# Performance work log

Hardware: AMD Instinct MI355X
Metric: run time of the kernel (lower is better)

The kernel has to match this reference:

```python
import jax, jax.numpy as jnp
import numpy as np

CONF_THR = 0.2      # confidence_threshold default
NMS_THR = 0.45      # nms_threshold default
TARGET_ID = 0       # NAME2ID['person'] in COCO ordering
CLASS_OFFSET = 1e4  # per-class box offset so cross-class IoU == 0 (per-class NMS)
B, N, C = 4, 8192, 80


def setup_inputs() -> dict:
    key = jax.random.key(0)
    kxy, kwh, kobj, kcls = jax.random.split(key, 4)
    xy = jax.random.uniform(kxy, (B, N, 2)) * 600.0          # x1, y1
    wh = jax.random.uniform(kwh, (B, N, 2)) * 100.0 + 1.0    # box w, h
    boxes = jnp.concatenate([xy, xy + wh], axis=-1)           # x1 y1 x2 y2
    obj = jax.random.uniform(kobj, (B, N, 1))                 # objectness score
    clsp = jax.random.uniform(kcls, (B, N, C))                # class probs
    detection = jnp.concatenate([boxes, obj, clsp], axis=-1)  # [B, N, 5+C]
    return {"detection": detection}


def _pairwise_iou(b):
    # b: [N, 4] in x1y1x2y2
    area = (b[:, 2] - b[:, 0]) * (b[:, 3] - b[:, 1])
    lt = jnp.maximum(b[:, None, :2], b[None, :, :2])
    rb = jnp.minimum(b[:, None, 2:], b[None, :, 2:])
    wh = jnp.clip(rb - lt, 0.0)
    inter = wh[..., 0] * wh[..., 1]
    return inter / (area[:, None] + area[None, :] - inter + 1e-9)


def _nms_image(boxes, scores, classprobs, labels):
    # Fixed-shape, masked equivalent of the torch per-image filter+per-class NMS.
    valid = (scores > CONF_THR) & (labels == TARGET_ID)
    s = jnp.where(valid, scores, -1.0)
    order = jnp.argsort(-s)  # descending score (NMS visiting order)
    b = boxes[order]
    s = s[order]
    cp = classprobs[order]
    lb = labels[order]
    v = valid[order]
    # Offset boxes per class label -> IoU between different classes is 0,
    # which exactly reproduces the per-class NMS loop.
    ob = b + lb.astype(b.dtype)[:, None] * CLASS_OFFSET
    iou = _pairwise_iou(ob)  # [N, N]

    def step(keep, xs):
        row, i, vi = xs
        suppressed = jnp.any(keep & (row > NMS_THR))
        k = vi & jnp.logical_not(suppressed)
        return keep.at[i].set(k), k

    _, keep = jax.lax.scan(
        step, jnp.zeros(s.shape[0], dtype=bool), (iou, jnp.arange(s.shape[0]), v)
    )
    # Compact kept detections to the front (stable sort preserves descending score
    # order among kept boxes, matching the final argsort in torch).
    s_rank = jnp.where(keep, s, -1.0)
    final = jnp.argsort(-s_rank)
    kf = keep[final]
    m = kf.astype(b.dtype)
    out_boxes = b[final] * m[:, None]
    out_scores = jnp.where(kf, s[final], 0.0)
    out_classprobs = cp[final] * m
    out_labels = jnp.where(kf, lb[final], -1)
    return out_boxes, out_scores, out_classprobs, out_labels


def reference(detection):
    # split_detections
    boxes = detection[..., :4]           # [B, N, 4]
    scores = detection[..., 4]           # [B, N]
    cls = detection[..., 5:]             # [B, N, C]
    classprobs = jnp.max(cls, axis=-1)
    labels = jnp.argmax(cls, axis=-1)
    # filter_detections, batched over images
    return jax.vmap(_nms_image)(boxes, scores, classprobs, labels)
```

## Files before the change

### kernel.cpp

```cpp
#include <hip/hip_runtime.h>
#include <cstdint>
#include <cstddef>

typedef unsigned long long u64;

#define BB 4
#define NN 8192
#define DSTRIDE 85
#define RPB 64
#define BPI 128
#define NBLK (BB * BPI)
#define RCAP 64
#define SCAP 192
#define CONF_THRF 0.2f
#define NMS_THRF 0.45f
#define PLANE (BB * NN)

__device__ __forceinline__ void wave_fence() {
  __asm__ volatile("s_waitcnt lgkmcnt(0)" ::: "memory");
  __builtin_amdgcn_wave_barrier();
}

__global__ __launch_bounds__(256) void scan_kernel(
    const float* __restrict__ det, float* __restrict__ out,
    int* __restrict__ counts, float* __restrict__ cand) {
  __shared__ int wcnt[4];
  const int tid = threadIdx.x;
  const int blk = blockIdx.x;
  const int r = tid >> 2, q = tid & 3;
  const int row = blk * RPB + r;
  const float* d = det + (size_t)row * DSTRIDE;

  float best = -1.0f; int barg = 0;
  const float* cb = d + 5 + 20 * q;
#pragma unroll
  for (int k = 0; k < 5; ++k) {
    float4 v = *reinterpret_cast<const float4*>(cb + 4 * k);
    int c0 = 20 * q + 4 * k;
    if (v.x > best) { best = v.x; barg = c0; }
    if (v.y > best) { best = v.y; barg = c0 + 1; }
    if (v.z > best) { best = v.z; barg = c0 + 2; }
    if (v.w > best) { best = v.w; barg = c0 + 3; }
  }
#pragma unroll
  for (int off = 1; off <= 2; off <<= 1) {
    float ov = __shfl_xor(best, off);
    int   oa = __shfl_xor(barg, off);
    if (ov > best || (ov == best && oa < barg)) { best = ov; barg = oa; }
  }

  float4 box = make_float4(0.f, 0.f, 0.f, 0.f);
  float score = 0.f;
  bool valid = false;
  if (q == 0) {
    box = *reinterpret_cast<const float4*>(d);
    score = d[4];
    valid = (score > CONF_THRF) && (barg == 0);
  }

  const int base = blk * RPB;
  if (tid < 64) {
    reinterpret_cast<float4*>(out)[base + tid] = make_float4(0.f, 0.f, 0.f, 0.f);
  } else if (tid < 128) {
    out[(size_t)PLANE * 4 + base + (tid - 64)] = 0.f;
  } else if (tid < 192) {
    out[(size_t)PLANE * 5 + base + (tid - 128)] = 0.f;
  } else {
    out[(size_t)PLANE * 6 + base + (tid - 192)] = -1.0f;
  }

  u64 mask = __ballot(valid);
  const int wave = tid >> 6, lane = tid & 63;
  if (lane == 0) wcnt[wave] = __popcll(mask);
  __syncthreads();
  if (valid) {
    int offw = (wave > 0 ? wcnt[0] : 0) + (wave > 1 ? wcnt[1] : 0) +
               (wave > 2 ? wcnt[2] : 0);
    int pos = __popcll(mask & ((1ull << lane) - 1ull));
    float* p = cand + ((size_t)blk * RCAP + (offw + pos)) * 8;
    reinterpret_cast<float4*>(p)[0] = box;
    reinterpret_cast<float4*>(p)[1] =
        make_float4(score, best, __int_as_float(row & (NN - 1)), 0.f);
  }
  if (tid == 0) counts[blk] = wcnt[0] + wcnt[1] + wcnt[2] + wcnt[3];
}

__global__ __launch_bounds__(64) void nms_kernel(
    float* __restrict__ out, const int* __restrict__ counts,
    const float* __restrict__ cand) {
  __shared__ u64 keys[SCAP];
  __shared__ u64 mat[SCAP * 3];
  __shared__ float ux1[SCAP], uy1[SCAP], ux2[SCAP], uy2[SCAP];
  __shared__ float usc[SCAP], ucp[SCAP];
  __shared__ float sx1[SCAP], sy1[SCAP], sx2[SCAP], sy2[SCAP];
  __shared__ float sar[SCAP], ssc[SCAP], scp[SCAP];

  const int img = blockIdx.x;
  const int lane = threadIdx.x;

  const int m0 = img * BPI + lane, m1 = m0 + 64;
  int c0 = counts[m0];
  int c1 = counts[m1];

  int s0 = c0;
#pragma unroll
  for (int d = 1; d < 64; d <<= 1) {
    int t = __shfl_up(s0, d);
    if (lane >= d) s0 += t;
  }
  int tot0 = __shfl(s0, 63);
  int s1 = c1;
#pragma unroll
  for (int d = 1; d < 64; d <<= 1) {
    int t = __shfl_up(s1, d);
    if (lane >= d) s1 += t;
  }
  s1 += tot0;
  int K = __shfl(s1, 63);
  if (K > SCAP) K = SCAP;
  int e0 = s0 - c0, e1 = s1 - c1;

#pragma unroll
  for (int pass = 0; pass < 2; ++pass) {
    int m = pass ? m1 : m0;
    int c = pass ? c1 : c0;
    int e = pass ? e1 : e0;
    const float4* p =
        reinterpret_cast<const float4*>(cand + (size_t)m * RCAP * 8);
    for (int k = 0; k < c; ++k) {
      int o = e + k;
      if (o < SCAP) {
        float4 a = p[2 * k], bq = p[2 * k + 1];
        ux1[o] = a.x; uy1[o] = a.y; ux2[o] = a.z; uy2[o] = a.w;
        usc[o] = bq.x; ucp[o] = bq.y;
        int idx = __float_as_int(bq.z);
        keys[o] = ((u64)__float_as_uint(bq.x) << 32) |
                  ((u64)(unsigned)(0xFFFF - idx) << 16) | (unsigned)o;
      }
    }
  }
  wave_fence();

  for (int o = lane; o < K; o += 64) {
    u64 my = keys[o];
    int rr = 0;
    for (int s = 0; s < K; ++s) rr += (keys[s] > my) ? 1 : 0;
    float x1 = ux1[o], y1 = uy1[o], x2 = ux2[o], y2 = uy2[o];
    sx1[rr] = x1; sy1[rr] = y1; sx2[rr] = x2; sy2[rr] = y2;
    sar[rr] = (x2 - x1) * (y2 - y1);
    ssc[rr] = usc[o]; scp[rr] = ucp[o];
  }
  wave_fence();

  for (int i = lane; i < K; i += 64) {
    float ax1 = sx1[i], ay1 = sy1[i], ax2 = sx2[i], ay2 = sy2[i], aa = sar[i];
    u64 w0 = 0, w1 = 0, w2 = 0;
    for (int j = i + 1; j < K; ++j) {
      float xx1 = fmaxf(ax1, sx1[j]);
      float yy1 = fmaxf(ay1, sy1[j]);
      float xx2 = fminf(ax2, sx2[j]);
      float yy2 = fminf(ay2, sy2[j]);
      float w = fmaxf(xx2 - xx1, 0.f);
      float h = fmaxf(yy2 - yy1, 0.f);
      float inter = w * h;
      float iou = inter / (aa + sar[j] - inter + 1e-9f);
      if (iou > NMS_THRF) {
        u64 bit = 1ull << (j & 63);
        int wj = j >> 6;
        w0 |= (wj == 0) ? bit : 0;
        w1 |= (wj == 1) ? bit : 0;
        w2 |= (wj == 2) ? bit : 0;
      }
    }
    mat[i * 3] = w0; mat[i * 3 + 1] = w1; mat[i * 3 + 2] = w2;
  }
  wave_fence();

  u64 rem0 = 0, rem1 = 0, rem2 = 0, kp0 = 0, kp1 = 0, kp2 = 0;
#define GREEDY_CHUNK(WW, REMW, KPW)                                      \
  for (int ii = 0; ii < 64; ++ii) {                                      \
    int i = (WW) * 64 + ii;                                              \
    if (i >= K) break;                                                   \
    u64 g0 = mat[i * 3], g1 = mat[i * 3 + 1], g2 = mat[i * 3 + 2];       \
    if (!((REMW >> ii) & 1ull)) {                                        \
      KPW |= 1ull << ii;                                                 \
      rem0 |= g0; rem1 |= g1; rem2 |= g2;                                \
    }                                                                    \
  }
  GREEDY_CHUNK(0, rem0, kp0)
  GREEDY_CHUNK(1, rem1, kp1)
  GREEDY_CHUNK(2, rem2, kp2)
#undef GREEDY_CHUNK

  for (int i = lane; i < K; i += 64) {
    int wi = i >> 6, bi = i & 63;
    u64 kw = (wi == 0) ? kp0 : (wi == 1) ? kp1 : kp2;
    if ((kw >> bi) & 1ull) {
      int rr = (wi > 0 ? __popcll(kp0) : 0) + (wi > 1 ? __popcll(kp1) : 0) +
               __popcll(kw & ((1ull << bi) - 1ull));
      size_t o = (size_t)img * NN + rr;
      reinterpret_cast<float4*>(out)[o] =
          make_float4(sx1[i], sy1[i], sx2[i], sy2[i]);
      out[(size_t)PLANE * 4 + o] = ssc[i];
      out[(size_t)PLANE * 5 + o] = scp[i];
      out[(size_t)PLANE * 6 + o] = 0.0f;
    }
  }
}

extern "C" void kernel_launch(void* const* d_in, const int* in_sizes, int n_in,
                              void* d_out, int out_size, void* d_ws, size_t ws_size,
                              hipStream_t stream) {
  const float* det = (const float*)d_in[0];
  float* out = (float*)d_out;
  int* counts = (int*)d_ws;
  float* cand = (float*)((char*)d_ws + 2048);

  scan_kernel<<<NBLK, 256, 0, stream>>>(det, out, counts, cand);
  nms_kernel<<<BB, 64, 0, stream>>>(out, counts, cand);
}
```

Baseline: 87.12 us.

## Stage detection rows in LDS with coalesced float4 loads, halve rows per block

The scan kernel now copies each block's contiguous slab of 32 detection rows into shared memory with fully coalesced float4 loads, then runs the per-row class argmax from LDS using 8 threads per row. Before, each thread read unaligned float4s directly from the 85-float-stride rows. Rows per block drop from 64 to 32, so the block count doubles to 1024, and the NMS kernel scans and gathers four count segments instead of two. This trades an extra LDS round trip and a barrier for better global-load coalescing and more parallelism. It also adds more candidate segments for the single-wave NMS gather to walk.

Result: slower. 89.57 us (+2.8%).

```diff
diff --git a/kernel.cpp b/kernel.cpp
--- a/kernel.cpp
+++ b/kernel.cpp
@@ -7,10 +7,10 @@
 #define BB 4
 #define NN 8192
 #define DSTRIDE 85
-#define RPB 64
-#define BPI 128
+#define RPB 32
+#define BPI 256
 #define NBLK (BB * BPI)
-#define RCAP 64
+#define RCAP 32
 #define SCAP 192
 #define CONF_THRF 0.2f
 #define NMS_THRF 0.45f
@@ -24,26 +24,33 @@
 __global__ __launch_bounds__(256) void scan_kernel(
     const float* __restrict__ det, float* __restrict__ out,
     int* __restrict__ counts, float* __restrict__ cand) {
+  __shared__ __align__(16) float st[RPB * DSTRIDE];
   __shared__ int wcnt[4];
   const int tid = threadIdx.x;
   const int blk = blockIdx.x;
-  const int r = tid >> 2, q = tid & 3;
-  const int row = blk * RPB + r;
-  const float* d = det + (size_t)row * DSTRIDE;
-
+
+  {
+    const float4* src =
+        reinterpret_cast<const float4*>(det + (size_t)blk * (RPB * DSTRIDE));
+    float4* dst = reinterpret_cast<float4*>(st);
+#pragma unroll
+    for (int i = 0; i < 3; ++i) {
+      int idx = tid + 256 * i;
+      if (idx < (RPB * DSTRIDE) / 4) dst[idx] = src[idx];
+    }
+  }
+  __syncthreads();
+
+  const int r = tid >> 3, o = tid & 7;
+  const float* rowp = st + r * DSTRIDE;
   float best = -1.0f; int barg = 0;
-  const float* cb = d + 5 + 20 * q;
 #pragma unroll
-  for (int k = 0; k < 5; ++k) {
-    float4 v = *reinterpret_cast<const float4*>(cb + 4 * k);
-    int c0 = 20 * q + 4 * k;
-    if (v.x > best) { best = v.x; barg = c0; }
-    if (v.y > best) { best = v.y; barg = c0 + 1; }
-    if (v.z > best) { best = v.z; barg = c0 + 2; }
-    if (v.w > best) { best = v.w; barg = c0 + 3; }
+  for (int k = 0; k < 10; ++k) {
+    float v = rowp[5 + 10 * o + k];
+    if (v > best) { best = v; barg = 10 * o + k; }
   }
 #pragma unroll
-  for (int off = 1; off <= 2; off <<= 1) {
+  for (int off = 1; off <= 4; off <<= 1) {
     float ov = __shfl_xor(best, off);
     int   oa = __shfl_xor(barg, off);
     if (ov > best || (ov == best && oa < barg)) { best = ov; barg = oa; }
@@ -52,21 +59,21 @@
   float4 box = make_float4(0.f, 0.f, 0.f, 0.f);
   float score = 0.f;
   bool valid = false;
-  if (q == 0) {
-    box = *reinterpret_cast<const float4*>(d);
-    score = d[4];
+  if (o == 0) {
+    box = make_float4(rowp[0], rowp[1], rowp[2], rowp[3]);
+    score = rowp[4];
     valid = (score > CONF_THRF) && (barg == 0);
   }
 
   const int base = blk * RPB;
-  if (tid < 64) {
+  if (tid < 32) {
     reinterpret_cast<float4*>(out)[base + tid] = make_float4(0.f, 0.f, 0.f, 0.f);
+  } else if (tid < 64) {
+    out[(size_t)PLANE * 4 + base + (tid - 32)] = 0.f;
+  } else if (tid < 96) {
+    out[(size_t)PLANE * 5 + base + (tid - 64)] = 0.f;
   } else if (tid < 128) {
-    out[(size_t)PLANE * 4 + base + (tid - 64)] = 0.f;
-  } else if (tid < 192) {
-    out[(size_t)PLANE * 5 + base + (tid - 128)] = 0.f;
-  } else {
-    out[(size_t)PLANE * 6 + base + (tid - 192)] = -1.0f;
+    out[(size_t)PLANE * 6 + base + (tid - 96)] = -1.0f;
   }
 
   u64 mask = __ballot(valid);
@@ -77,10 +84,11 @@
     int offw = (wave > 0 ? wcnt[0] : 0) + (wave > 1 ? wcnt[1] : 0) +
                (wave > 2 ? wcnt[2] : 0);
     int pos = __popcll(mask & ((1ull << lane) - 1ull));
-    float* p = cand + ((size_t)blk * RCAP + (offw + pos)) * 8;
-    reinterpret_cast<float4*>(p)[0] = box;
-    reinterpret_cast<float4*>(p)[1] =
-        make_float4(score, best, __int_as_float(row & (NN - 1)), 0.f);
+    float4* p =
+        reinterpret_cast<float4*>(cand + ((size_t)blk * RCAP + offw + pos) * 8);
+    p[0] = box;
+    p[1] = make_float4(score, best,
+                       __int_as_float((blk & (BPI - 1)) * RPB + r), 0.f);
   }
   if (tid == 0) counts[blk] = wcnt[0] + wcnt[1] + wcnt[2] + wcnt[3];
 }
@@ -97,58 +105,65 @@
 
   const int img = blockIdx.x;
   const int lane = threadIdx.x;
-
-  const int m0 = img * BPI + lane, m1 = m0 + 64;
-  int c0 = counts[m0];
-  int c1 = counts[m1];
-
-  int s0 = c0;
-#pragma unroll
-  for (int d = 1; d < 64; d <<= 1) {
-    int t = __shfl_up(s0, d);
-    if (lane >= d) s0 += t;
-  }
-  int tot0 = __shfl(s0, 63);
-  int s1 = c1;
-#pragma unroll
-  for (int d = 1; d < 64; d <<= 1) {
-    int t = __shfl_up(s1, d);
-    if (lane >= d) s1 += t;
-  }
-  s1 += tot0;
-  int K = __shfl(s1, 63);
+  const int mbase = img * BPI + lane;
+
+  int c0 = counts[mbase];
+  int c1 = counts[mbase + 64];
+  int c2 = counts[mbase + 128];
+  int c3 = counts[mbase + 192];
+
+  int running = 0;
+  int e0, e1, e2, e3;
+#define SCAN_SEG(CC, EE)                                \
+  {                                                     \
+    int s = CC;                                         \
+    _Pragma("unroll")                                   \
+    for (int d = 1; d < 64; d <<= 1) {                  \
+      int t = __shfl_up(s, d);                          \
+      if (lane >= d) s += t;                            \
+    }                                                   \
+    EE = running + s - CC;                              \
+    running += __shfl(s, 63);                           \
+  }
+  SCAN_SEG(c0, e0)
+  SCAN_SEG(c1, e1)
+  SCAN_SEG(c2, e2)
+  SCAN_SEG(c3, e3)
+#undef SCAN_SEG
+  int K = running;
   if (K > SCAP) K = SCAP;
-  int e0 = s0 - c0, e1 = s1 - c1;
-
-#pragma unroll
-  for (int pass = 0; pass < 2; ++pass) {
-    int m = pass ? m1 : m0;
-    int c = pass ? c1 : c0;
-    int e = pass ? e1 : e0;
-    const float4* p =
-        reinterpret_cast<const float4*>(cand + (size_t)m * RCAP * 8);
-    for (int k = 0; k < c; ++k) {
-      int o = e + k;
-      if (o < SCAP) {
-        float4 a = p[2 * k], bq = p[2 * k + 1];
-        ux1[o] = a.x; uy1[o] = a.y; ux2[o] = a.z; uy2[o] = a.w;
-        usc[o] = bq.x; ucp[o] = bq.y;
-        int idx = __float_as_int(bq.z);
-        keys[o] = ((u64)__float_as_uint(bq.x) << 32) |
-                  ((u64)(unsigned)(0xFFFF - idx) << 16) | (unsigned)o;
-      }
-    }
-  }
+
+#define GATHER_SEG(PP, CC, EE)                                               \
+  {                                                                          \
+    const float4* p = reinterpret_cast<const float4*>(                       \
+        cand + (size_t)(mbase + 64 * (PP)) * RCAP * 8);                      \
+    for (int k = 0; k < CC; ++k) {                                           \
+      int oo = EE + k;                                                       \
+      if (oo < SCAP) {                                                       \
+        float4 a = p[2 * k], bq = p[2 * k + 1];                              \
+        ux1[oo] = a.x; uy1[oo] = a.y; ux2[oo] = a.z; uy2[oo] = a.w;          \
+        usc[oo] = bq.x; ucp[oo] = bq.y;                                      \
+        int idx = __float_as_int(bq.z);                                      \
+        keys[oo] = ((u64)__float_as_uint(bq.x) << 32) |                      \
+                   ((u64)(unsigned)(0xFFFF - idx) << 16) | (unsigned)oo;     \
+      }                                                                      \
+    }                                                                        \
+  }
+  GATHER_SEG(0, c0, e0)
+  GATHER_SEG(1, c1, e1)
+  GATHER_SEG(2, c2, e2)
+  GATHER_SEG(3, c3, e3)
+#undef GATHER_SEG
   wave_fence();
 
-  for (int o = lane; o < K; o += 64) {
-    u64 my = keys[o];
+  for (int oo = lane; oo < K; oo += 64) {
+    u64 my = keys[oo];
     int rr = 0;
     for (int s = 0; s < K; ++s) rr += (keys[s] > my) ? 1 : 0;
-    float x1 = ux1[o], y1 = uy1[o], x2 = ux2[o], y2 = uy2[o];
+    float x1 = ux1[oo], y1 = uy1[oo], x2 = ux2[oo], y2 = uy2[oo];
     sx1[rr] = x1; sy1[rr] = y1; sx2[rr] = x2; sy2[rr] = y2;
     sar[rr] = (x2 - x1) * (y2 - y1);
-    ssc[rr] = usc[o]; scp[rr] = ucp[o];
+    ssc[rr] = usc[oo]; scp[rr] = ucp[oo];
   }
   wave_fence();
 
@@ -198,12 +213,12 @@
     if ((kw >> bi) & 1ull) {
       int rr = (wi > 0 ? __popcll(kp0) : 0) + (wi > 1 ? __popcll(kp1) : 0) +
                __popcll(kw & ((1ull << bi) - 1ull));
-      size_t o = (size_t)img * NN + rr;
-      reinterpret_cast<float4*>(out)[o] =
+      size_t oo = (size_t)img * NN + rr;
+      reinterpret_cast<float4*>(out)[oo] =
           make_float4(sx1[i], sy1[i], sx2[i], sy2[i]);
-      out[(size_t)PLANE * 4 + o] = ssc[i];
-      out[(size_t)PLANE * 5 + o] = scp[i];
-      out[(size_t)PLANE * 6 + o] = 0.0f;
+      out[(size_t)PLANE * 4 + oo] = ssc[i];
+      out[(size_t)PLANE * 5 + oo] = scp[i];
+      out[(size_t)PLANE * 6 + oo] = 0.0f;
     }
   }
 }
@@ -214,7 +229,7 @@
   const float* det = (const float*)d_in[0];
   float* out = (float*)d_out;
   int* counts = (int*)d_ws;
-  float* cand = (float*)((char*)d_ws + 2048);
+  float* cand = (float*)((char*)d_ws + 4096);
 
   scan_kernel<<<NBLK, 256, 0, stream>>>(det, out, counts, cand);
   nms_kernel<<<BB, 64, 0, stream>>>(out, counts, cand);
```
